# Performance work log

Hardware: AMD Instinct MI355X
Metric: run time of the kernel (lower is better)

The kernel has to match this reference:

```python
import jax, jax.numpy as jnp
import numpy as np
import math

L_S = 64  # segment length (factor)


def setup_inputs() -> dict:
    key = jax.random.key(0)
    kq, kk, kv = jax.random.split(key, 3)
    B, L, H, D = 4, 8192, 16, 64
    return {
        "queries": jax.random.normal(kq, (B, L, H, D), dtype=jnp.float32),
        "keys": jax.random.normal(kk, (B, L, H, D), dtype=jnp.float32),
        "values": jax.random.normal(kv, (B, L, H, D), dtype=jnp.float32),
        "attn_mask": 0,
    }


def reference(queries, keys, values, attn_mask):
    B, L, H, D = queries.shape
    Ls = L_S
    M = L // Ls  # L % Ls == 0 by construction, so addition_Q path is a no-op
    scale = 1.0 / math.sqrt(Ls * D)

    # segment: [B, M, Ls, H, D]
    sq = queries.reshape(B, M, Ls, H, D)
    sk = keys.reshape(B, M, Ls, H, D)
    sv = values.reshape(B, M, Ls, H, D)

    # rfft over head dim D, ortho norm -> [B, M, Ls, H, D//2+1] complex
    qf = jnp.fft.rfft(sq, axis=-1, norm="ortho")
    kf = jnp.fft.rfft(sk, axis=-1, norm="ortho")
    vf = jnp.fft.rfft(sv, axis=-1, norm="ortho")

    # complex segment correlation: [B, H, M, M]
    scores = jnp.einsum("bmlhd,bnlhd->bhmn", qf, jnp.conj(kf)) / math.sqrt(D)
    A = jax.nn.softmax(scale * jnp.abs(scores), axis=-1)  # real
    Ac = A.astype(qf.dtype)  # complex with zero imaginary part

    # complex weighted sum of value spectra: [B, M, Ls, H, D//2+1]
    Vf = jnp.einsum("bhmn,bnlhd->bmlhd", Ac, vf)
    V = jnp.fft.irfft(Vf, n=D, axis=-1, norm="ortho")  # real [B, M, Ls, H, D]
    return V.reshape(B, L, H, D)
```

## Files before the change

### kernel.cpp

```cpp
#include <hip/hip_runtime.h>
#include <cstdint>
#include <cstddef>


typedef short bf16x8 __attribute__((ext_vector_type(8)));
typedef float f32x4 __attribute__((ext_vector_type(4)));

__device__ __forceinline__ ushort f2bf(float f) {
    union { float f; uint32_t u; } v; v.f = f;
    uint32_t r = (v.u + 0x7FFFu + ((v.u >> 16) & 1u)) >> 16;
    return (ushort)r;
}

__device__ __forceinline__ float bf2f(ushort h) {
    union { uint32_t u; float f; } v; v.u = ((uint32_t)h) << 16;
    return v.f;
}

__global__ void k_gmat(ushort* __restrict__ GimH, ushort* __restrict__ GimL) {
    const float lam = 1.0f / 32768.0f;
    const float c = 3.14159265358979323846f / 32.0f;
    for (int e = threadIdx.x + blockIdx.x * blockDim.x; e < 4096; e += blockDim.x * gridDim.x) {
        int d = e >> 6, dp = e & 63;
        int delta = d - dp;
        float im = 0.f;
        for (int k = 0; k <= 32; ++k) {
            int r = ((k * delta) % 64 + 64) % 64;
            im -= sinf(c * (float)r);
        }
        im *= lam;
        ushort ih = f2bf(im);
        GimH[e] = ih;
        GimL[e] = f2bf(im - bf2f(ih));
    }
}

#define PSCALE 0.17677669529663687f

__global__ __launch_bounds__(256) void k_prep_q(const float* __restrict__ Q, ushort* __restrict__ Qf) {
    int t = threadIdx.x;
    for (int it = 0; it < 8; ++it) {
        int g = blockIdx.x * 8 + it;
        int bh = g >> 7, m = g & 127;
        int b = bh >> 4, h = bh & 15;
        const float* qbase = Q + ((size_t)(b * 8192 + m * 64)) * 1024 + h * 64;
        ushort* obase = Qf + ((size_t)bh * 128 + m) * 4224;
        #pragma unroll
        for (int k = 0; k < 4; ++k) {
            int idx = k * 256 + t;
            int l = idx >> 4, d4 = (idx & 15) * 4;
            float4 v = *(const float4*)(qbase + (size_t)l * 1024 + d4);
            ushort4 o; o.x = f2bf(v.x); o.y = f2bf(v.y); o.z = f2bf(v.z); o.w = f2bf(v.w);
            *(ushort4*)(obase + l * 64 + d4) = o;
            float pe = v.x + v.z, po = v.y + v.w;
            pe += __shfl_xor(pe, 1); po += __shfl_xor(po, 1);
            pe += __shfl_xor(pe, 2); po += __shfl_xor(po, 2);
            pe += __shfl_xor(pe, 4); po += __shfl_xor(po, 4);
            pe += __shfl_xor(pe, 8); po += __shfl_xor(po, 8);
            if ((t & 15) == 0) {
                ushort2 pp; pp.x = f2bf(pe * PSCALE); pp.y = f2bf(po * PSCALE);
                *(ushort2*)(obase + 4096 + 2 * l) = pp;
            }
        }
    }
}

__global__ __launch_bounds__(256) void k_prep_k(const float* __restrict__ K,
                                                const ushort* __restrict__ GimH,
                                                const ushort* __restrict__ GimL,
                                                ushort* __restrict__ Kf, ushort* __restrict__ Kim) {
    __shared__ ushort kb[64 * 72];
    int t = threadIdx.x;
    int lane = t & 63, wave = t >> 6;
    int wm = wave >> 1, wn = wave & 1;
    int row16 = lane & 15, quad = lane >> 4;
    int rrow = t >> 2, rcol = (t & 3) * 16;

    bf16x8 gih[2][2], gil[2][2];
    #pragma unroll
    for (int nt = 0; nt < 2; ++nt)
        #pragma unroll
        for (int kk = 0; kk < 2; ++kk) {
            int off = (wn * 32 + nt * 16 + row16) * 64 + kk * 32 + quad * 8;
            gih[nt][kk] = *(const bf16x8*)(GimH + off);
            gil[nt][kk] = *(const bf16x8*)(GimL + off);
        }

    for (int it = 0; it < 8; ++it) {
        int g = blockIdx.x * 8 + it;
        int bh = g >> 7, n = g & 127;
        int b = bh >> 4, h = bh & 15;
        const float* kbase = K + ((size_t)(b * 8192 + n * 64 + rrow)) * 1024 + h * 64 + rcol;
        ushort* kfrow = Kf + ((size_t)bh * 128 + n) * 4224;
        float pe = 0.f, po = 0.f;
        #pragma unroll
        for (int c = 0; c < 4; ++c) {
            float4 v = *(const float4*)(kbase + c * 4);
            ushort4 o; o.x = f2bf(v.x); o.y = f2bf(v.y); o.z = f2bf(v.z); o.w = f2bf(v.w);
            *(ushort4*)&kb[rrow * 72 + rcol + c * 4] = o;
            *(ushort4*)(kfrow + rrow * 64 + rcol + c * 4) = o;
            pe += v.x + v.z; po += v.y + v.w;
        }
        pe += __shfl_xor(pe, 1); po += __shfl_xor(po, 1);
        pe += __shfl_xor(pe, 2); po += __shfl_xor(po, 2);
        if ((t & 3) == 0) {
            ushort2 pp; pp.x = f2bf(pe * PSCALE); pp.y = f2bf(po * PSCALE);
            *(ushort2*)(kfrow + 4096 + 2 * rrow) = pp;
        }
        __syncthreads();

        f32x4 acc[2][2] = {};
        #pragma unroll
        for (int kk = 0; kk < 2; ++kk) {
            bf16x8 a[2];
            #pragma unroll
            for (int mt = 0; mt < 2; ++mt)
                a[mt] = *(const bf16x8*)&kb[(wm * 32 + mt * 16 + row16) * 72 + kk * 32 + quad * 8];
            #pragma unroll
            for (int mt = 0; mt < 2; ++mt)
                #pragma unroll
                for (int nt = 0; nt < 2; ++nt) {
                    acc[mt][nt] = __builtin_amdgcn_mfma_f32_16x16x32_bf16(a[mt], gih[nt][kk], acc[mt][nt], 0, 0, 0);
                    acc[mt][nt] = __builtin_amdgcn_mfma_f32_16x16x32_bf16(a[mt], gil[nt][kk], acc[mt][nt], 0, 0, 0);
                }
        }
        __syncthreads();
        #pragma unroll
        for (int mt = 0; mt < 2; ++mt)
            #pragma unroll
            for (int nt = 0; nt < 2; ++nt)
                #pragma unroll
                for (int i = 0; i < 4; ++i)
                    kb[(wm * 32 + mt * 16 + quad * 4 + i) * 72 + wn * 32 + nt * 16 + row16] = f2bf(acc[mt][nt][i]);
        __syncthreads();
        ushort* kimrow = Kim + ((size_t)bh * 128 + n) * 4096;
        *(uint4*)(kimrow + rrow * 64 + rcol)     = *(uint4*)&kb[rrow * 72 + rcol];
        *(uint4*)(kimrow + rrow * 64 + rcol + 8) = *(uint4*)&kb[rrow * 72 + rcol + 8];
        __syncthreads();
    }
}

__global__ __launch_bounds__(256) void k_scores(const ushort* __restrict__ Qf,
                                                const ushort* __restrict__ Kf,
                                                const ushort* __restrict__ Kim,
                                                float* __restrict__ Sre, float* __restrict__ Sim) {
    __shared__ ushort qt[64 * 72], ret[64 * 72], imt[64 * 72];
    int bh = blockIdx.y;
    int mh = blockIdx.x >> 1, nh = blockIdx.x & 1;
    int m0 = mh * 64, n0 = nh * 64;
    int t = threadIdx.x;
    int lane = t & 63, wave = t >> 6;
    int wm = wave >> 1, wn = wave & 1;
    int row16 = lane & 15, quad = lane >> 4;
    const ushort* qg = Qf + ((size_t)bh * 128 + m0) * 4224;
    const ushort* rg = Kf + ((size_t)bh * 128 + n0) * 4224;
    const ushort* ig = Kim + ((size_t)bh * 128 + n0) * 4096;
    uint4 rq[2], rk[2], ri[2];
    #pragma unroll
    for (int p = 0; p < 2; ++p) {
        int idx = p * 256 + t;
        int row = idx >> 3, ch = idx & 7;
        rq[p] = *(const uint4*)(qg + (size_t)row * 4224 + ch * 8);
        rk[p] = *(const uint4*)(rg + (size_t)row * 4224 + ch * 8);
        ri[p] = *(const uint4*)(ig + (size_t)row * 4096 + ch * 8);
    }
    f32x4 accre[2][2] = {};
    f32x4 accim[2][2] = {};
    for (int kt = 0; kt < 66; ++kt) {
        bool haveim = kt < 64;
        #pragma unroll
        for (int p = 0; p < 2; ++p) {
            int idx = p * 256 + t;
            int row = idx >> 3, ch = idx & 7;
            int lo = row * 72 + ch * 8;
            *(uint4*)&qt[lo] = rq[p];
            *(uint4*)&ret[lo] = rk[p];
            if (haveim) *(uint4*)&imt[lo] = ri[p];
        }
        __syncthreads();
        if (kt + 1 < 66) {
            int j0 = (kt + 1) * 64;
            #pragma unroll
            for (int p = 0; p < 2; ++p) {
                int idx = p * 256 + t;
                int row = idx >> 3, ch = idx & 7;
                rq[p] = *(const uint4*)(qg + (size_t)row * 4224 + j0 + ch * 8);
                rk[p] = *(const uint4*)(rg + (size_t)row * 4224 + j0 + ch * 8);
                if (kt + 1 < 64) ri[p] = *(const uint4*)(ig + (size_t)row * 4096 + j0 + ch * 8);
            }
        }
        #pragma unroll
        for (int kk = 0; kk < 2; ++kk) {
            bf16x8 a[2], br[2], bi[2];
            #pragma unroll
            for (int mt = 0; mt < 2; ++mt)
                a[mt] = *(const bf16x8*)&qt[(wm * 32 + mt * 16 + row16) * 72 + kk * 32 + quad * 8];
            #pragma unroll
            for (int nt = 0; nt < 2; ++nt) {
                br[nt] = *(const bf16x8*)&ret[(wn * 32 + nt * 16 + row16) * 72 + kk * 32 + quad * 8];
                if (haveim) bi[nt] = *(const bf16x8*)&imt[(wn * 32 + nt * 16 + row16) * 72 + kk * 32 + quad * 8];
            }
            #pragma unroll
            for (int mt = 0; mt < 2; ++mt)
                #pragma unroll
                for (int nt = 0; nt < 2; ++nt) {
                    accre[mt][nt] = __builtin_amdgcn_mfma_f32_16x16x32_bf16(a[mt], br[nt], accre[mt][nt], 0, 0, 0);
                    if (haveim)
                        accim[mt][nt] = __builtin_amdgcn_mfma_f32_16x16x32_bf16(a[mt], bi[nt], accim[mt][nt], 0, 0, 0);
                }
        }
        __syncthreads();
    }
    float* sre = Sre + (size_t)bh * 16384;
    float* sim = Sim + (size_t)bh * 16384;
    #pragma unroll
    for (int mt = 0; mt < 2; ++mt)
        #pragma unroll
        for (int nt = 0; nt < 2; ++nt)
            #pragma unroll
            for (int i = 0; i < 4; ++i) {
                int r = m0 + wm * 32 + mt * 16 + quad * 4 + i;
                int c = n0 + wn * 32 + nt * 16 + row16;
                sre[r * 128 + c] = accre[mt][nt][i] * 0.0009765625f;
                sim[r * 128 + c] = accim[mt][nt][i];
            }
}

__global__ __launch_bounds__(256) void k_softmax(const float* __restrict__ Sre,
                                                 const float* __restrict__ Sim,
                                                 ushort* __restrict__ A) {
    int t = threadIdx.x;
    int lane = t & 63, wave = t >> 6;
    for (int it = 0; it < 4; ++it) {
        int row = blockIdx.x * 16 + it * 4 + wave;
        size_t off = (size_t)row * 128 + lane * 2;
        float2 re = *(const float2*)(Sre + off);
        float2 im = *(const float2*)(Sim + off);
        float lg0 = sqrtf(re.x * re.x + im.x * im.x);
        float lg1 = sqrtf(re.y * re.y + im.y * im.y);
        float mx = fmaxf(lg0, lg1);
        for (int o = 32; o > 0; o >>= 1) mx = fmaxf(mx, __shfl_xor(mx, o));
        float e0 = expf(lg0 - mx), e1 = expf(lg1 - mx);
        float s = e0 + e1;
        for (int o = 32; o > 0; o >>= 1) s += __shfl_xor(s, o);
        float inv = 1.0f / s;
        ushort2 o2; o2.x = f2bf(e0 * inv); o2.y = f2bf(e1 * inv);
        *(ushort2*)(A + off) = o2;
    }
}

__global__ __launch_bounds__(256) void k_vt(const float* __restrict__ V, ushort* __restrict__ Vt) {
    __shared__ float tile[64 * 68];
    int lg = blockIdx.x, nh = blockIdx.y, bh = blockIdx.z;
    int b = bh >> 4, h = bh & 15;
    int t = threadIdx.x;
    int n = t & 63, dq = t >> 6;
    int d = t >> 2, cq = t & 3;
    for (int it = 0; it < 4; ++it) {
        int l = lg * 4 + it;
        const float* vbase = V + ((size_t)(b * 8192 + (nh * 64 + n) * 64 + l)) * 1024 + h * 64;
        #pragma unroll
        for (int r = 0; r < 4; ++r) {
            int d0 = r * 16 + dq * 4;
            float4 v = *(const float4*)(vbase + d0);
            tile[(d0 + 0) * 68 + n] = v.x; tile[(d0 + 1) * 68 + n] = v.y;
            tile[(d0 + 2) * 68 + n] = v.z; tile[(d0 + 3) * 68 + n] = v.w;
        }
        __syncthreads();
        __align__(16) ushort u[16];
        #pragma unroll
        for (int i = 0; i < 16; ++i) u[i] = f2bf(tile[d * 68 + cq * 16 + i]);
        ushort* ob = Vt + ((size_t)bh * 4096 + l * 64 + d) * 128 + nh * 64 + cq * 16;
        *(uint4*)(ob) = *(uint4*)&u[0];
        *(uint4*)(ob + 8) = *(uint4*)&u[8];
        __syncthreads();
    }
}

__global__ __launch_bounds__(256) void k_mix(const ushort* __restrict__ A,
                                             const ushort* __restrict__ Vt,
                                             float* __restrict__ Out) {
    __shared__ ushort At[128 * 136], Vtl[64 * 136];
    int grp = blockIdx.x, bh = blockIdx.y;
    int b = bh >> 4, h = bh & 15;
    int t = threadIdx.x;
    int lane = t & 63, wave = t >> 6;
    int row16 = lane & 15, quad = lane >> 4;
    const ushort* ag = A + (size_t)bh * 16384;
    #pragma unroll
    for (int p = 0; p < 8; ++p) {
        int idx = p * 256 + t;
        int row = idx >> 4, ch = idx & 15;
        *(uint4*)&At[row * 136 + ch * 8] = *(const uint4*)(ag + row * 128 + ch * 8);
    }
    for (int jt8 = 0; jt8 < 8; ++jt8) {
        int jt = grp * 8 + jt8;
        int j0 = jt * 64;
        const ushort* vg = Vt + ((size_t)bh * 4096 + j0) * 128;
        __syncthreads();
        #pragma unroll
        for (int p = 0; p < 4; ++p) {
            int idx = p * 256 + t;
            int row = idx >> 4, ch = idx & 15;
            *(uint4*)&Vtl[row * 136 + ch * 8] = *(const uint4*)(vg + (size_t)row * 128 + ch * 8);
        }
        __syncthreads();
        f32x4 acc[2][4] = {};
        #pragma unroll
        for (int kk = 0; kk < 4; ++kk) {
            bf16x8 a[2], bv[4];
            #pragma unroll
            for (int mt = 0; mt < 2; ++mt)
                a[mt] = *(const bf16x8*)&At[(wave * 32 + mt * 16 + row16) * 136 + kk * 32 + quad * 8];
            #pragma unroll
            for (int j2 = 0; j2 < 4; ++j2)
                bv[j2] = *(const bf16x8*)&Vtl[(j2 * 16 + row16) * 136 + kk * 32 + quad * 8];
            #pragma unroll
            for (int mt = 0; mt < 2; ++mt)
                #pragma unroll
                for (int j2 = 0; j2 < 4; ++j2)
                    acc[mt][j2] = __builtin_amdgcn_mfma_f32_16x16x32_bf16(a[mt], bv[j2], acc[mt][j2], 0, 0, 0);
        }
        #pragma unroll
        for (int mt = 0; mt < 2; ++mt)
            #pragma unroll
            for (int j2 = 0; j2 < 4; ++j2)
                #pragma unroll
                for (int i = 0; i < 4; ++i) {
                    int m = wave * 32 + mt * 16 + quad * 4 + i;
                    int dd = j2 * 16 + row16;
                    Out[((size_t)(b * 8192 + m * 64 + jt)) * 1024 + h * 64 + dd] = acc[mt][j2][i];
                }
    }
}

extern "C" void kernel_launch(void* const* d_in, const int* in_sizes, int n_in,
                              void* d_out, int out_size, void* d_ws, size_t ws_size,
                              hipStream_t stream) {
    const float* Q = (const float*)d_in[0];
    const float* K = (const float*)d_in[1];
    const float* V = (const float*)d_in[2];
    float* Out = (float*)d_out;
    char* ws = (char*)d_ws;
    ushort* GimH = (ushort*)ws;
    ushort* GimL = GimH + 4096;
    float* Sre  = (float*)(ws + 32768);
    float* Sim  = (float*)(ws + 32768 + 4194304);
    ushort* A   = (ushort*)(ws + 32768 + 2 * 4194304);
    ushort* Qf  = (ushort*)(ws + 32768 + 2 * 4194304 + 2097152);
    ushort* Kf  = Qf + (size_t)64 * 128 * 4224;
    ushort* Kim = Kf + (size_t)64 * 128 * 4224;
    ushort* Vt  = Qf;

    k_gmat<<<16, 256, 0, stream>>>(GimH, GimL);
    k_prep_q<<<1024, 256, 0, stream>>>(Q, Qf);
    k_prep_k<<<1024, 256, 0, stream>>>(K, GimH, GimL, Kf, Kim);
    k_scores<<<dim3(4, 64), 256, 0, stream>>>(Qf, Kf, Kim, Sre, Sim);
    k_softmax<<<512, 256, 0, stream>>>(Sre, Sim, A);
    k_vt<<<dim3(16, 2, 64), 256, 0, stream>>>(V, Vt);
    k_mix<<<dim3(8, 64), 256, 0, stream>>>(A, Vt, Out);
}
```

Measured before the change: 645.3 us.

## Split-K scores GEMM into 4 partial slices, drop LDS staging, widen mix grid

The scores kernel now splits the long 4224-element reduction into four slices, each handled by its own block, and writes partial real and imaginary sums to separate buffers. The softmax kernel adds those partials back together. Each wave now loads its MFMA operands directly from global memory instead of staging them through shared memory with barriers. The mix kernel grid is doubled, with each block handling half as many tiles. The aim is more blocks in flight (1024 instead of 256), since the old grid was too small to fill the GPU. The cost is extra partial-sum traffic and uncoalesced direct global loads.

```diff
diff --git a/kernel.cpp b/kernel.cpp
--- a/kernel.cpp
+++ b/kernel.cpp
@@ -140,112 +140,106 @@
     }
 }
 
-__global__ __launch_bounds__(256) void k_scores(const ushort* __restrict__ Qf,
-                                                const ushort* __restrict__ Kf,
-                                                const ushort* __restrict__ Kim,
-                                                float* __restrict__ Sre, float* __restrict__ Sim) {
-    __shared__ ushort qt[64 * 72], ret[64 * 72], imt[64 * 72];
-    int bh = blockIdx.y;
-    int mh = blockIdx.x >> 1, nh = blockIdx.x & 1;
+__global__ __launch_bounds__(256, 4) void k_scores(const ushort* __restrict__ Qf,
+                                                   const ushort* __restrict__ Kf,
+                                                   const ushort* __restrict__ Kim,
+                                                   float* __restrict__ SreP, float* __restrict__ SimP) {
+    int qid = blockIdx.x;
+    int s = blockIdx.y;
+    int bh = blockIdx.z;
+    int mh = qid >> 1, nh = qid & 1;
     int m0 = mh * 64, n0 = nh * 64;
     int t = threadIdx.x;
     int lane = t & 63, wave = t >> 6;
     int wm = wave >> 1, wn = wave & 1;
-    int row16 = lane & 15, quad = lane >> 4;
-    const ushort* qg = Qf + ((size_t)bh * 128 + m0) * 4224;
-    const ushort* rg = Kf + ((size_t)bh * 128 + n0) * 4224;
-    const ushort* ig = Kim + ((size_t)bh * 128 + n0) * 4096;
-    uint4 rq[2], rk[2], ri[2];
-    #pragma unroll
-    for (int p = 0; p < 2; ++p) {
-        int idx = p * 256 + t;
-        int row = idx >> 3, ch = idx & 7;
-        rq[p] = *(const uint4*)(qg + (size_t)row * 4224 + ch * 8);
-        rk[p] = *(const uint4*)(rg + (size_t)row * 4224 + ch * 8);
-        ri[p] = *(const uint4*)(ig + (size_t)row * 4096 + ch * 8);
-    }
+    int row16 = lane & 15, ql = lane >> 4;
+
+    const ushort* aB = Qf + ((size_t)(bh * 128 + m0 + wm * 32 + row16)) * 4224 + ql * 8;
+    const ushort* bB = Kf + ((size_t)(bh * 128 + n0 + wn * 32 + row16)) * 4224 + ql * 8;
+    const ushort* iB = Kim + ((size_t)(bh * 128 + n0 + wn * 32 + row16)) * 4096 + ql * 8;
+
     f32x4 accre[2][2] = {};
     f32x4 accim[2][2] = {};
-    for (int kt = 0; kt < 66; ++kt) {
-        bool haveim = kt < 64;
-        #pragma unroll
-        for (int p = 0; p < 2; ++p) {
-            int idx = p * 256 + t;
-            int row = idx >> 3, ch = idx & 7;
-            int lo = row * 72 + ch * 8;
-            *(uint4*)&qt[lo] = rq[p];
-            *(uint4*)&ret[lo] = rk[p];
-            if (haveim) *(uint4*)&imt[lo] = ri[p];
-        }
-        __syncthreads();
-        if (kt + 1 < 66) {
-            int j0 = (kt + 1) * 64;
-            #pragma unroll
-            for (int p = 0; p < 2; ++p) {
-                int idx = p * 256 + t;
-                int row = idx >> 3, ch = idx & 7;
-                rq[p] = *(const uint4*)(qg + (size_t)row * 4224 + j0 + ch * 8);
-                rk[p] = *(const uint4*)(rg + (size_t)row * 4224 + j0 + ch * 8);
-                if (kt + 1 < 64) ri[p] = *(const uint4*)(ig + (size_t)row * 4096 + j0 + ch * 8);
+    int c0 = s * 1024;
+    for (int k6 = 0; k6 < 16; ++k6) {
+        int co = c0 + k6 * 64;
+        bf16x8 a[2][2], b[2][2], bi[2][2];
+        #pragma unroll
+        for (int kk = 0; kk < 2; ++kk)
+            #pragma unroll
+            for (int x = 0; x < 2; ++x) {
+                a[kk][x]  = *(const bf16x8*)(aB + (size_t)x * 16 * 4224 + co + kk * 32);
+                b[kk][x]  = *(const bf16x8*)(bB + (size_t)x * 16 * 4224 + co + kk * 32);
+                bi[kk][x] = *(const bf16x8*)(iB + (size_t)x * 16 * 4096 + co + kk * 32);
             }
-        }
-        #pragma unroll
-        for (int kk = 0; kk < 2; ++kk) {
-            bf16x8 a[2], br[2], bi[2];
-            #pragma unroll
-            for (int mt = 0; mt < 2; ++mt)
-                a[mt] = *(const bf16x8*)&qt[(wm * 32 + mt * 16 + row16) * 72 + kk * 32 + quad * 8];
-            #pragma unroll
-            for (int nt = 0; nt < 2; ++nt) {
-                br[nt] = *(const bf16x8*)&ret[(wn * 32 + nt * 16 + row16) * 72 + kk * 32 + quad * 8];
-                if (haveim) bi[nt] = *(const bf16x8*)&imt[(wn * 32 + nt * 16 + row16) * 72 + kk * 32 + quad * 8];
+        #pragma unroll
+        for (int kk = 0; kk < 2; ++kk)
+            #pragma unroll
+            for (int mt = 0; mt < 2; ++mt)
+                #pragma unroll
+                for (int nt = 0; nt < 2; ++nt) {
+                    accre[mt][nt] = __builtin_amdgcn_mfma_f32_16x16x32_bf16(a[kk][mt], b[kk][nt], accre[mt][nt], 0, 0, 0);
+                    accim[mt][nt] = __builtin_amdgcn_mfma_f32_16x16x32_bf16(a[kk][mt], bi[kk][nt], accim[mt][nt], 0, 0, 0);
+                }
+    }
+    if (s < 2) {
+        int co = (64 + s) * 64;
+        bf16x8 a[2][2], b[2][2];
+        #pragma unroll
+        for (int kk = 0; kk < 2; ++kk)
+            #pragma unroll
+            for (int x = 0; x < 2; ++x) {
+                a[kk][x] = *(const bf16x8*)(aB + (size_t)x * 16 * 4224 + co + kk * 32);
+                b[kk][x] = *(const bf16x8*)(bB + (size_t)x * 16 * 4224 + co + kk * 32);
             }
-            #pragma unroll
-            for (int mt = 0; mt < 2; ++mt)
-                #pragma unroll
-                for (int nt = 0; nt < 2; ++nt) {
-                    accre[mt][nt] = __builtin_amdgcn_mfma_f32_16x16x32_bf16(a[mt], br[nt], accre[mt][nt], 0, 0, 0);
-                    if (haveim)
-                        accim[mt][nt] = __builtin_amdgcn_mfma_f32_16x16x32_bf16(a[mt], bi[nt], accim[mt][nt], 0, 0, 0);
-                }
-        }
-        __syncthreads();
-    }
-    float* sre = Sre + (size_t)bh * 16384;
-    float* sim = Sim + (size_t)bh * 16384;
+        #pragma unroll
+        for (int kk = 0; kk < 2; ++kk)
+            #pragma unroll
+            for (int mt = 0; mt < 2; ++mt)
+                #pragma unroll
+                for (int nt = 0; nt < 2; ++nt)
+                    accre[mt][nt] = __builtin_amdgcn_mfma_f32_16x16x32_bf16(a[kk][mt], b[kk][nt], accre[mt][nt], 0, 0, 0);
+    }
+    float* sre = SreP + (size_t)s * 1048576 + (size_t)(bh * 128) * 128;
+    float* sim = SimP + (size_t)s * 1048576 + (size_t)(bh * 128) * 128;
     #pragma unroll
     for (int mt = 0; mt < 2; ++mt)
         #pragma unroll
         for (int nt = 0; nt < 2; ++nt)
             #pragma unroll
             for (int i = 0; i < 4; ++i) {
-                int r = m0 + wm * 32 + mt * 16 + quad * 4 + i;
+                int r = m0 + wm * 32 + mt * 16 + ql * 4 + i;
                 int c = n0 + wn * 32 + nt * 16 + row16;
                 sre[r * 128 + c] = accre[mt][nt][i] * 0.0009765625f;
                 sim[r * 128 + c] = accim[mt][nt][i];
             }
 }
 
-__global__ __launch_bounds__(256) void k_softmax(const float* __restrict__ Sre,
-                                                 const float* __restrict__ Sim,
+__global__ __launch_bounds__(256) void k_softmax(const float* __restrict__ SreP,
+                                                 const float* __restrict__ SimP,
                                                  ushort* __restrict__ A) {
     int t = threadIdx.x;
     int lane = t & 63, wave = t >> 6;
     for (int it = 0; it < 4; ++it) {
         int row = blockIdx.x * 16 + it * 4 + wave;
-        size_t off = (size_t)row * 128 + lane * 2;
-        float2 re = *(const float2*)(Sre + off);
-        float2 im = *(const float2*)(Sim + off);
-        float lg0 = sqrtf(re.x * re.x + im.x * im.x);
-        float lg1 = sqrtf(re.y * re.y + im.y * im.y);
+        size_t base = (size_t)row * 128 + lane * 2;
+        float re0 = 0.f, re1 = 0.f, im0 = 0.f, im1 = 0.f;
+        #pragma unroll
+        for (int s = 0; s < 4; ++s) {
+            float2 r = *(const float2*)(SreP + (size_t)s * 1048576 + base);
+            float2 m2 = *(const float2*)(SimP + (size_t)s * 1048576 + base);
+            re0 += r.x; re1 += r.y; im0 += m2.x; im1 += m2.y;
+        }
+        float lg0 = sqrtf(re0 * re0 + im0 * im0);
+        float lg1 = sqrtf(re1 * re1 + im1 * im1);
         float mx = fmaxf(lg0, lg1);
         for (int o = 32; o > 0; o >>= 1) mx = fmaxf(mx, __shfl_xor(mx, o));
         float e0 = expf(lg0 - mx), e1 = expf(lg1 - mx);
-        float s = e0 + e1;
-        for (int o = 32; o > 0; o >>= 1) s += __shfl_xor(s, o);
-        float inv = 1.0f / s;
+        float sum = e0 + e1;
+        for (int o = 32; o > 0; o >>= 1) sum += __shfl_xor(sum, o);
+        float inv = 1.0f / sum;
         ushort2 o2; o2.x = f2bf(e0 * inv); o2.y = f2bf(e1 * inv);
-        *(ushort2*)(A + off) = o2;
+        *(ushort2*)(A + base) = o2;
     }
 }
 
@@ -293,8 +287,8 @@
         int row = idx >> 4, ch = idx & 15;
         *(uint4*)&At[row * 136 + ch * 8] = *(const uint4*)(ag + row * 128 + ch * 8);
     }
-    for (int jt8 = 0; jt8 < 8; ++jt8) {
-        int jt = grp * 8 + jt8;
+    for (int jt4 = 0; jt4 < 4; ++jt4) {
+        int jt = grp * 4 + jt4;
         int j0 = jt * 64;
         const ushort* vg = Vt + ((size_t)bh * 4096 + j0) * 128;
         __syncthreads();
@@ -344,10 +338,10 @@
     char* ws = (char*)d_ws;
     ushort* GimH = (ushort*)ws;
     ushort* GimL = GimH + 4096;
-    float* Sre  = (float*)(ws + 32768);
-    float* Sim  = (float*)(ws + 32768 + 4194304);
-    ushort* A   = (ushort*)(ws + 32768 + 2 * 4194304);
-    ushort* Qf  = (ushort*)(ws + 32768 + 2 * 4194304 + 2097152);
+    float* SreP = (float*)(ws + 32768);
+    float* SimP = SreP + (size_t)4 * 1048576;
+    ushort* A   = (ushort*)(ws + 32768 + (size_t)2 * 16777216);
+    ushort* Qf  = A + 1048576;
     ushort* Kf  = Qf + (size_t)64 * 128 * 4224;
     ushort* Kim = Kf + (size_t)64 * 128 * 4224;
     ushort* Vt  = Qf;
@@ -355,8 +349,8 @@
     k_gmat<<<16, 256, 0, stream>>>(GimH, GimL);
     k_prep_q<<<1024, 256, 0, stream>>>(Q, Qf);
     k_prep_k<<<1024, 256, 0, stream>>>(K, GimH, GimL, Kf, Kim);
-    k_scores<<<dim3(4, 64), 256, 0, stream>>>(Qf, Kf, Kim, Sre, Sim);
-    k_softmax<<<512, 256, 0, stream>>>(Sre, Sim, A);
+    k_scores<<<dim3(4, 4, 64), 256, 0, stream>>>(Qf, Kf, Kim, SreP, SimP);
+    k_softmax<<<512, 256, 0, stream>>>(SreP, SimP, A);
     k_vt<<<dim3(16, 2, 64), 256, 0, stream>>>(V, Vt);
-    k_mix<<<dim3(8, 64), 256, 0, stream>>>(A, Vt, Out);
-}
+    k_mix<<<dim3(16, 64), 256, 0, stream>>>(A, Vt, Out);
+}
```

Result: faster. 572.6 us (-11.3%).
